# Optimization experiments

Measured on AMD Instinct MI355X. Metric: run time of the kernel, lower is better.

Reference implementation:

```python
import jax, jax.numpy as jnp
import numpy as np

H = 16          # num_attention_heads
D = 1024        # hidden_size
HD = D // H     # attention_head_size = 64


def setup_inputs() -> dict:
    key = jax.random.key(0)
    ks = jax.random.split(key, 9)
    s = 1.0 / np.sqrt(D)
    return {
        "hidden_states": jax.random.normal(ks[0], (4, 1024, D), jnp.float32),
        "encoder_hidden_states": jax.random.normal(ks[1], (4, 1024, D), jnp.float32),
        "attention_mask": jnp.zeros((4, 1, 1, 2048), jnp.float32),
        "Wq": jax.random.normal(ks[2], (D, D), jnp.float32) * s,
        "bq": jnp.zeros((D,), jnp.float32),
        "Wk": jax.random.normal(ks[3], (D, D), jnp.float32) * s,
        "bk": jnp.zeros((D,), jnp.float32),
        "Wv": jax.random.normal(ks[4], (D, D), jnp.float32) * s,
        "bv": jnp.zeros((D,), jnp.float32),
    }


def _split_heads(x):
    # [B, S, D] -> [B, H, S, HD]
    B, S, _ = x.shape
    return x.reshape(B, S, H, HD).transpose(0, 2, 1, 3)


def reference(hidden_states, encoder_hidden_states, attention_mask, Wq, bq, Wk, bk, Wv, bv):
    # KV over concat(encoder, decoder); Q over decoder hidden states only.
    all_hidden = jnp.concatenate([encoder_hidden_states, hidden_states], axis=1)  # [B, Skv, D]
    q = _split_heads(hidden_states @ Wq + bq)        # [B, H, Sq, HD]
    k = _split_heads(all_hidden @ Wk + bk)           # [B, H, Skv, HD]
    v = _split_heads(all_hidden @ Wv + bv)           # [B, H, Skv, HD]

    scores = jnp.einsum("bhqd,bhkd->bhqk", q, k) / np.sqrt(HD).astype(np.float32)
    scores = scores + attention_mask                 # additive mask, broadcast
    probs = jax.nn.softmax(scores, axis=-1)          # dropout p=0 (eval)
    ctx = jnp.einsum("bhqk,bhkd->bhqd", probs, v)    # [B, H, Sq, HD]
    B, _, Sq, _ = ctx.shape
    return ctx.transpose(0, 2, 1, 3).reshape(B, Sq, D)
```

## Files before the change

### kernel.cpp

```cpp
#include <hip/hip_runtime.h>


typedef _Float16 f16;
typedef __attribute__((ext_vector_type(4))) _Float16 half4;
typedef __attribute__((ext_vector_type(8))) _Float16 half8;
typedef __attribute__((ext_vector_type(4))) float floatx4;
typedef __attribute__((ext_vector_type(16))) float floatx16;
typedef __attribute__((ext_vector_type(4))) unsigned int uint4v;

#define GLOAD16(gp, lp)                                                        \
    __builtin_amdgcn_global_load_lds(                                          \
        (const __attribute__((address_space(1))) void*)(gp),                   \
        (__attribute__((address_space(3))) void*)(lp), 16, 0, 0)

__global__ void prep_kernel(const float* __restrict__ hid, const float* __restrict__ enc,
                            const float* __restrict__ Wq, const float* __restrict__ Wk,
                            const float* __restrict__ Wv, f16* __restrict__ Wtq,
                            f16* __restrict__ Wtk, f16* __restrict__ Wtv,
                            f16* __restrict__ Aall) {
    int bid = blockIdx.x, tid = threadIdx.x;
    if (bid < 3072) {
        __shared__ float tile[32][33];
        int z = bid >> 10, xy = bid & 1023;
        const float* W = (z == 0) ? Wq : (z == 1) ? Wk : Wv;
        f16* Wt = (z == 0) ? Wtq : (z == 1) ? Wtk : Wtv;
        int n0 = (xy & 31) * 32, k0 = (xy >> 5) * 32;
        int tx = tid & 31, ty = tid >> 5;
        #pragma unroll
        for (int i = 0; i < 32; i += 8)
            tile[ty + i][tx] = W[(k0 + ty + i) * 1024 + n0 + tx];
        __syncthreads();
        #pragma unroll
        for (int i = 0; i < 32; i += 8)
            Wt[(n0 + ty + i) * 1024 + k0 + tx] = (f16)tile[tx][ty + i];
    } else {
        int t = (bid - 3072) * 256 + tid;
        int rowg = t >> 7, col = (t & 127) * 8;
        int b = rowg >> 11, r = rowg & 2047;
        const float* src = (r < 1024 ? enc + ((size_t)b * 1024 + r) * 1024
                                     : hid + ((size_t)b * 1024 + (r - 1024)) * 1024) + col;
        float4 v0 = *(const float4*)src, v1 = *(const float4*)(src + 4);
        half8 o;
        o[0] = (f16)v0.x; o[1] = (f16)v0.y; o[2] = (f16)v0.z; o[3] = (f16)v0.w;
        o[4] = (f16)v1.x; o[5] = (f16)v1.y; o[6] = (f16)v1.z; o[7] = (f16)v1.w;
        *(half8*)(Aall + (size_t)rowg * 1024 + col) = o;
    }
}

__launch_bounds__(256)
__global__ void qkv_gemm(const f16* __restrict__ Aall,
                         const f16* __restrict__ Wtq, const f16* __restrict__ Wtk,
                         const f16* __restrict__ Wtv,
                         const float* __restrict__ bq, const float* __restrict__ bk,
                         const float* __restrict__ bv,
                         f16* __restrict__ Qw, f16* __restrict__ Kw, f16* __restrict__ Vtw) {
    int mode = blockIdx.z;
    if (mode == 0 && blockIdx.x >= 32) return;
    __shared__ f16 As[2][128 * 32];
    __shared__ f16 Bs[2][128 * 32];

    const f16* Wt = (mode == 0) ? Wtq : (mode == 1) ? Wtk : Wtv;
    const float* bias = (mode == 0) ? bq : (mode == 1) ? bk : bv;
    f16* out = (mode == 0) ? Qw : (mode == 1) ? Kw : Vtw;

    int tid = threadIdx.x;
    int m0 = blockIdx.x * 128, n0 = blockIdx.y * 128;
    int wid = tid >> 6, lane = tid & 63;
    int wm = (wid >> 1) * 64, wn = (wid & 1) * 64;
    int lr = lane & 15, lg = lane >> 4;

    floatx4 acc[4][4];
    #pragma unroll
    for (int i = 0; i < 4; i++)
        #pragma unroll
        for (int j = 0; j < 4; j++) acc[i][j] = (floatx4)(0.f);

    int trow = tid >> 2, tcol = (tid & 3) * 8;
    const f16 *a0g, *a1g;
    {
        int mA0 = m0 + trow, mA1 = mA0 + 64;
        if (mode == 0) {
            int b0 = mA0 >> 10, b1 = mA1 >> 10;
            a0g = Aall + ((size_t)(b0 * 2048 + 1024 + (mA0 & 1023))) * 1024 + tcol;
            a1g = Aall + ((size_t)(b1 * 2048 + 1024 + (mA1 & 1023))) * 1024 + tcol;
        } else {
            a0g = Aall + (size_t)mA0 * 1024 + tcol;
            a1g = Aall + (size_t)mA1 * 1024 + tcol;
        }
    }
    const f16* b0g = Wt + (size_t)(n0 + trow) * 1024 + tcol;
    const f16* b1g = Wt + (size_t)(n0 + trow + 64) * 1024 + tcol;

    GLOAD16(a0g, &As[0][tid * 8]);
    GLOAD16(a1g, &As[0][tid * 8 + 2048]);
    GLOAD16(b0g, &Bs[0][tid * 8]);
    GLOAD16(b1g, &Bs[0][tid * 8 + 2048]);
    __syncthreads();

    int cur = 0;
    for (int k0 = 0; k0 < 1024; k0 += 32) {
        if (k0 < 992) {
            int nx = cur ^ 1;
            GLOAD16(a0g + k0 + 32, &As[nx][tid * 8]);
            GLOAD16(a1g + k0 + 32, &As[nx][tid * 8 + 2048]);
            GLOAD16(b0g + k0 + 32, &Bs[nx][tid * 8]);
            GLOAD16(b1g + k0 + 32, &Bs[nx][tid * 8 + 2048]);
        }
        half8 a[4], bf[4];
        #pragma unroll
        for (int i = 0; i < 4; i++)
            a[i] = *(const half8*)&As[cur][(wm + i * 16 + lr) * 32 + lg * 8];
        #pragma unroll
        for (int j = 0; j < 4; j++)
            bf[j] = *(const half8*)&Bs[cur][(wn + j * 16 + lr) * 32 + lg * 8];
        __builtin_amdgcn_s_setprio(1);
        #pragma unroll
        for (int i = 0; i < 4; i++)
            #pragma unroll
            for (int j = 0; j < 4; j++)
                acc[i][j] = __builtin_amdgcn_mfma_f32_16x16x32_f16(a[i], bf[j], acc[i][j], 0, 0, 0);
        __builtin_amdgcn_s_setprio(0);
        __syncthreads();
        cur ^= 1;
    }

    if (mode == 2) {
        #pragma unroll
        for (int i = 0; i < 4; i++) {
            int mbase = m0 + wm + i * 16 + lg * 4;
            int b = mbase >> 11, s = mbase & 2047;
            #pragma unroll
            for (int j = 0; j < 4; j++) {
                int n = n0 + wn + j * 16 + lr;
                int h = n >> 6, d = n & 63;
                float bv = bias[n];
                half4 w;
                #pragma unroll
                for (int r = 0; r < 4; r++) w[r] = (f16)(acc[i][j][r] + bv);
                *(half4*)(out + ((size_t)((b * 16 + h) * 64 + d)) * 2048 + s) = w;
            }
        }
    } else {
        int Sout = (mode == 0) ? 1024 : 2048;
        #pragma unroll
        for (int i = 0; i < 4; i++) {
            int mbase = m0 + wm + i * 16 + lg * 4;
            #pragma unroll
            for (int j = 0; j < 4; j++) {
                int n = n0 + wn + j * 16 + lr;
                int h = n >> 6, d = n & 63;
                float bv = bias[n];
                #pragma unroll
                for (int r = 0; r < 4; r++) {
                    int m = mbase + r;
                    int b = (mode == 0) ? (m >> 10) : (m >> 11);
                    int s = (mode == 0) ? (m & 1023) : (m & 2047);
                    out[((size_t)(b * 16 + h) * Sout + s) * 64 + d] = (f16)(acc[i][j][r] + bv);
                }
            }
        }
    }
}

__device__ inline half8 pack_swap(float s0, float s1, float s2, float s3,
                                  float s4, float s5, float s6, float s7) {
    unsigned a0 = __builtin_bit_cast(unsigned, __builtin_amdgcn_cvt_pkrtz(s0, s1));
    unsigned b0 = __builtin_bit_cast(unsigned, __builtin_amdgcn_cvt_pkrtz(s4, s5));
    unsigned a1 = __builtin_bit_cast(unsigned, __builtin_amdgcn_cvt_pkrtz(s2, s3));
    unsigned b1 = __builtin_bit_cast(unsigned, __builtin_amdgcn_cvt_pkrtz(s6, s7));
    asm("v_permlane32_swap_b32 %0, %1" : "+v"(a0), "+v"(b0));
    asm("v_permlane32_swap_b32 %0, %1" : "+v"(a1), "+v"(b1));
    uint4v w = {a0, a1, b0, b1};
    return __builtin_bit_cast(half8, w);
}

__device__ inline half8 pack_noswap(float s0, float s1, float s2, float s3,
                                    float s4, float s5, float s6, float s7) {
    unsigned w0 = __builtin_bit_cast(unsigned, __builtin_amdgcn_cvt_pkrtz(s0, s1));
    unsigned w1 = __builtin_bit_cast(unsigned, __builtin_amdgcn_cvt_pkrtz(s2, s3));
    unsigned w2 = __builtin_bit_cast(unsigned, __builtin_amdgcn_cvt_pkrtz(s4, s5));
    unsigned w3 = __builtin_bit_cast(unsigned, __builtin_amdgcn_cvt_pkrtz(s6, s7));
    uint4v w = {w0, w1, w2, w3};
    return __builtin_bit_cast(half8, w);
}

__launch_bounds__(256)
__global__ void attn_kernel(const f16* __restrict__ Q, const f16* __restrict__ K,
                            const f16* __restrict__ Vt, const float* __restrict__ mask,
                            float* __restrict__ out) {
    __shared__ f16 Kt[2][64 * 72];
    __shared__ f16 Vtt[2][64 * 72];
    __shared__ float maskLds[2048];

    const float LOG2E = 1.4426950408889634f;
    int tid = threadIdx.x;
    int wid = tid >> 6, lane = tid & 63;
    int l31 = lane & 31, l5 = lane >> 5;

    int bid = blockIdx.x + 8 * blockIdx.y;
    int xcd = bid & 7, w = bid >> 3;
    int bh = xcd * 8 + (w >> 3);
    int xblk = w & 7;
    int b = bh >> 4;
    int q = xblk * 128 + wid * 32 + l31;

    half8 pa, pcode;
    #pragma unroll
    for (int j = 0; j < 8; j++) { pa[j] = (f16)0; pcode[j] = (f16)(8 * l5 + j); }
    if (l31 < 16 && (l31 >> 3) == l5) pa[l31 & 7] = (f16)1;
    floatx16 pd = __builtin_amdgcn_mfma_f32_32x32x16_f16(pa, pcode, (floatx16)0.f, 0, 0, 0);
    float r4 = __shfl(pd[0], 32);
    bool twoblk = (r4 > 6.0f);

    const float* maskp = mask + b * 2048;
    for (int i = tid; i < 512; i += 256) {
        float4 mv = ((const float4*)maskp)[i];
        mv.x = mv.x * LOG2E - 8.0f; mv.y = mv.y * LOG2E - 8.0f;
        mv.z = mv.z * LOG2E - 8.0f; mv.w = mv.w * LOG2E - 8.0f;
        ((float4*)maskLds)[i] = mv;
    }

    const f16* qrow = Q + ((size_t)bh * 1024 + q) * 64;
    half8 qf[4];
    if (!twoblk) {
        #pragma unroll
        for (int ks = 0; ks < 4; ks++)
            qf[ks] = *(const half8*)(qrow + ks * 16 + l5 * 8);
    } else {
        #pragma unroll
        for (int ks = 0; ks < 4; ks++) {
            half4 lo = *(const half4*)(qrow + ks * 16 + 4 * l5);
            half4 hi = *(const half4*)(qrow + ks * 16 + 8 + 4 * l5);
            qf[ks][0] = lo[0]; qf[ks][1] = lo[1]; qf[ks][2] = lo[2]; qf[ks][3] = lo[3];
            qf[ks][4] = hi[0]; qf[ks][5] = hi[1]; qf[ks][6] = hi[2]; qf[ks][7] = hi[3];
        }
    }
    const f16 qs = (f16)(0.125f * 1.4426950408889634f);
    #pragma unroll
    for (int ks = 0; ks < 4; ks++)
        #pragma unroll
        for (int x = 0; x < 8; x++) qf[ks][x] *= qs;

    half8 aones;
    #pragma unroll
    for (int j = 0; j < 8; j++) aones[j] = (l31 == 0) ? (f16)1 : (f16)0;

    floatx16 o0 = (floatx16)0.f, o1 = (floatx16)0.f, o2 = (floatx16)0.f;

    int sr = tid >> 2, sc = (tid & 3) * 16;
    const f16* Ksrc = K + ((size_t)bh * 2048 + sr) * 64 + sc;
    const f16* Vsrc = Vt + ((size_t)(bh * 64 + sr)) * 2048 + sc;

    half8 rk0 = *(const half8*)(Ksrc);
    half8 rk1 = *(const half8*)(Ksrc + 8);
    half8 rv0 = *(const half8*)(Vsrc);
    half8 rv1 = *(const half8*)(Vsrc + 8);
    *(half8*)&Kt[0][sr * 72 + sc]      = rk0;
    *(half8*)&Kt[0][sr * 72 + sc + 8]  = rk1;
    *(half8*)&Vtt[0][sr * 72 + sc]     = rv0;
    *(half8*)&Vtt[0][sr * 72 + sc + 8] = rv1;
    rk0 = *(const half8*)(Ksrc + (size_t)64 * 64);
    rk1 = *(const half8*)(Ksrc + (size_t)64 * 64 + 8);
    rv0 = *(const half8*)(Vsrc + 64);
    rv1 = *(const half8*)(Vsrc + 64 + 8);
    __syncthreads();

    int cur = 0;
    for (int kv0 = 0; kv0 < 2048; kv0 += 64) {
        if (kv0 < 2048 - 64) {
            int nx = cur ^ 1;
            *(half8*)&Kt[nx][sr * 72 + sc]      = rk0;
            *(half8*)&Kt[nx][sr * 72 + sc + 8]  = rk1;
            *(half8*)&Vtt[nx][sr * 72 + sc]     = rv0;
            *(half8*)&Vtt[nx][sr * 72 + sc + 8] = rv1;
            if (kv0 < 2048 - 128) {
                rk0 = *(const half8*)(Ksrc + (size_t)(kv0 + 128) * 64);
                rk1 = *(const half8*)(Ksrc + (size_t)(kv0 + 128) * 64 + 8);
                rv0 = *(const half8*)(Vsrc + kv0 + 128);
                rv1 = *(const half8*)(Vsrc + kv0 + 128 + 8);
            }
        }

        floatx16 sf0, sf1;
        #pragma unroll
        for (int g = 0; g < 4; g++) {
            float4 mk0 = *(const float4*)&maskLds[kv0 + 8 * g + 4 * l5];
            float4 mk1 = *(const float4*)&maskLds[kv0 + 32 + 8 * g + 4 * l5];
            #pragma unroll
            for (int i = 0; i < 4; i++) {
                sf0[4 * g + i] = ((const float*)&mk0)[i];
                sf1[4 * g + i] = ((const float*)&mk1)[i];
            }
        }

        __builtin_amdgcn_s_setprio(1);
        #pragma unroll
        for (int ks = 0; ks < 4; ks++) {
            half8 k0 = *(const half8*)&Kt[cur][l31 * 72 + ks * 16 + l5 * 8];
            half8 k1 = *(const half8*)&Kt[cur][(32 + l31) * 72 + ks * 16 + l5 * 8];
            sf0 = __builtin_amdgcn_mfma_f32_32x32x16_f16(k0, qf[ks], sf0, 0, 0, 0);
            sf1 = __builtin_amdgcn_mfma_f32_32x32x16_f16(k1, qf[ks], sf1, 0, 0, 0);
        }
        __builtin_amdgcn_s_setprio(0);

        #pragma unroll
        for (int r = 0; r < 16; r++) {
            sf0[r] = exp2f(sf0[r]);
            sf1[r] = exp2f(sf1[r]);
        }

        half8 pb[4];
        if (!twoblk) {
            pb[0] = pack_swap(sf0[0], sf0[1], sf0[2], sf0[3], sf0[4], sf0[5], sf0[6], sf0[7]);
            pb[1] = pack_swap(sf0[8], sf0[9], sf0[10], sf0[11], sf0[12], sf0[13], sf0[14], sf0[15]);
            pb[2] = pack_swap(sf1[0], sf1[1], sf1[2], sf1[3], sf1[4], sf1[5], sf1[6], sf1[7]);
            pb[3] = pack_swap(sf1[8], sf1[9], sf1[10], sf1[11], sf1[12], sf1[13], sf1[14], sf1[15]);
        } else {
            pb[0] = pack_noswap(sf0[0], sf0[1], sf0[2], sf0[3], sf0[4], sf0[5], sf0[6], sf0[7]);
            pb[1] = pack_noswap(sf0[8], sf0[9], sf0[10], sf0[11], sf0[12], sf0[13], sf0[14], sf0[15]);
            pb[2] = pack_noswap(sf1[0], sf1[1], sf1[2], sf1[3], sf1[4], sf1[5], sf1[6], sf1[7]);
            pb[3] = pack_noswap(sf1[8], sf1[9], sf1[10], sf1[11], sf1[12], sf1[13], sf1[14], sf1[15]);
        }

        __builtin_amdgcn_s_setprio(1);
        #pragma unroll
        for (int kb = 0; kb < 4; kb++) {
            half8 v0 = *(const half8*)&Vtt[cur][l31 * 72 + kb * 16 + l5 * 8];
            half8 v1 = *(const half8*)&Vtt[cur][(32 + l31) * 72 + kb * 16 + l5 * 8];
            o0 = __builtin_amdgcn_mfma_f32_32x32x16_f16(v0, pb[kb], o0, 0, 0, 0);
            o1 = __builtin_amdgcn_mfma_f32_32x32x16_f16(v1, pb[kb], o1, 0, 0, 0);
            o2 = __builtin_amdgcn_mfma_f32_32x32x16_f16(aones, pb[kb], o2, 0, 0, 0);
        }
        __builtin_amdgcn_s_setprio(0);

        asm volatile("s_waitcnt lgkmcnt(0)" ::: "memory");
        __builtin_amdgcn_sched_barrier(0);
        __builtin_amdgcn_s_barrier();
        cur ^= 1;
    }

    float l_all = __shfl(o2[0], l31);
    int h = bh & 15;
    float inv = 1.f / l_all;
    float* orow = out + ((size_t)(b * 1024 + q)) * 1024 + h * 64;
    #pragma unroll
    for (int g = 0; g < 4; g++) {
        float4 r0 = {o0[4 * g] * inv, o0[4 * g + 1] * inv, o0[4 * g + 2] * inv, o0[4 * g + 3] * inv};
        float4 r1 = {o1[4 * g] * inv, o1[4 * g + 1] * inv, o1[4 * g + 2] * inv, o1[4 * g + 3] * inv};
        *(float4*)&orow[8 * g + 4 * l5]      = r0;
        *(float4*)&orow[32 + 8 * g + 4 * l5] = r1;
    }
}

extern "C" void kernel_launch(void* const* d_in, const int* in_sizes, int n_in,
                              void* d_out, int out_size, void* d_ws, size_t ws_size,
                              hipStream_t stream) {
    const float* hid  = (const float*)d_in[0];
    const float* enc  = (const float*)d_in[1];
    const float* mask = (const float*)d_in[2];
    const float* Wq   = (const float*)d_in[3];
    const float* bq   = (const float*)d_in[4];
    const float* Wk   = (const float*)d_in[5];
    const float* bk   = (const float*)d_in[6];
    const float* Wv   = (const float*)d_in[7];
    const float* bv   = (const float*)d_in[8];
    float* out = (float*)d_out;

    char* ws = (char*)d_ws;
    f16* Wtq  = (f16*)(ws + ((size_t)0 << 20));
    f16* Wtk  = (f16*)(ws + ((size_t)2 << 20));
    f16* Wtv  = (f16*)(ws + ((size_t)4 << 20));
    f16* Aall = (f16*)(ws + ((size_t)6 << 20));
    f16* Qw   = (f16*)(ws + ((size_t)22 << 20));
    f16* Kw   = (f16*)(ws + ((size_t)30 << 20));
    f16* Vtw  = (f16*)(ws + ((size_t)46 << 20));

    prep_kernel<<<7168, 256, 0, stream>>>(hid, enc, Wq, Wk, Wv, Wtq, Wtk, Wtv, Aall);

    qkv_gemm<<<dim3(64, 8, 3), 256, 0, stream>>>(Aall, Wtq, Wtk, Wtv, bq, bk, bv, Qw, Kw, Vtw);

    attn_kernel<<<dim3(8, 64), 256, 0, stream>>>(Qw, Kw, Vtw, mask, out);
}
```

Baseline: 146.7 us.

## Swizzle QKV GEMM LDS tiles and keep two loads in flight with explicit waitcnt

Reworks the QKV projection GEMM main loop to unroll by two over separate LDS buffers. Loads are issued two stages ahead, with hand-placed s_waitcnt vmcnt and raw barriers replacing __syncthreads, so one tile's global-to-LDS copy overlaps compute on the other. It also XOR-swizzles the 16-byte column chunk on both the LDS write and read sides to cut LDS bank conflicts on the fragment reads. The manual wait counts rely on exact ordering of memory operations and could expose races if the compiler reorders them.

```diff
diff --git a/kernel.cpp b/kernel.cpp
--- a/kernel.cpp
+++ b/kernel.cpp
@@ -56,8 +56,10 @@
                          f16* __restrict__ Qw, f16* __restrict__ Kw, f16* __restrict__ Vtw) {
     int mode = blockIdx.z;
     if (mode == 0 && blockIdx.x >= 32) return;
-    __shared__ f16 As[2][128 * 32];
-    __shared__ f16 Bs[2][128 * 32];
+    __shared__ f16 As0[128 * 32];
+    __shared__ f16 Bs0[128 * 32];
+    __shared__ f16 As1[128 * 32];
+    __shared__ f16 Bs1[128 * 32];
 
     const f16* Wt = (mode == 0) ? Wtq : (mode == 1) ? Wtk : Wtv;
     const float* bias = (mode == 0) ? bq : (mode == 1) ? bk : bv;
@@ -75,7 +77,8 @@
         #pragma unroll
         for (int j = 0; j < 4; j++) acc[i][j] = (floatx4)(0.f);
 
-    int trow = tid >> 2, tcol = (tid & 3) * 8;
+    int trow = tid >> 2;
+    int tcol = (((tid & 3) ^ ((tid >> 3) & 3))) * 8;
     const f16 *a0g, *a1g;
     {
         int mA0 = m0 + trow, mA1 = mA0 + 64;
@@ -91,38 +94,66 @@
     const f16* b0g = Wt + (size_t)(n0 + trow) * 1024 + tcol;
     const f16* b1g = Wt + (size_t)(n0 + trow + 64) * 1024 + tcol;
 
-    GLOAD16(a0g, &As[0][tid * 8]);
-    GLOAD16(a1g, &As[0][tid * 8 + 2048]);
-    GLOAD16(b0g, &Bs[0][tid * 8]);
-    GLOAD16(b1g, &Bs[0][tid * 8 + 2048]);
-    __syncthreads();
-
-    int cur = 0;
-    for (int k0 = 0; k0 < 1024; k0 += 32) {
-        if (k0 < 992) {
-            int nx = cur ^ 1;
-            GLOAD16(a0g + k0 + 32, &As[nx][tid * 8]);
-            GLOAD16(a1g + k0 + 32, &As[nx][tid * 8 + 2048]);
-            GLOAD16(b0g + k0 + 32, &Bs[nx][tid * 8]);
-            GLOAD16(b1g + k0 + 32, &Bs[nx][tid * 8 + 2048]);
-        }
-        half8 a[4], bf[4];
-        #pragma unroll
-        for (int i = 0; i < 4; i++)
-            a[i] = *(const half8*)&As[cur][(wm + i * 16 + lr) * 32 + lg * 8];
-        #pragma unroll
-        for (int j = 0; j < 4; j++)
-            bf[j] = *(const half8*)&Bs[cur][(wn + j * 16 + lr) * 32 + lg * 8];
-        __builtin_amdgcn_s_setprio(1);
-        #pragma unroll
-        for (int i = 0; i < 4; i++)
-            #pragma unroll
-            for (int j = 0; j < 4; j++)
-                acc[i][j] = __builtin_amdgcn_mfma_f32_16x16x32_f16(a[i], bf[j], acc[i][j], 0, 0, 0);
-        __builtin_amdgcn_s_setprio(0);
-        __syncthreads();
-        cur ^= 1;
-    }
+    int rcol = (lg ^ ((lr >> 1) & 3)) * 8;
+
+    GLOAD16(a0g, &As0[tid * 8]);
+    GLOAD16(a1g, &As0[tid * 8 + 2048]);
+    GLOAD16(b0g, &Bs0[tid * 8]);
+    GLOAD16(b1g, &Bs0[tid * 8 + 2048]);
+    GLOAD16(a0g + 32, &As1[tid * 8]);
+    GLOAD16(a1g + 32, &As1[tid * 8 + 2048]);
+    GLOAD16(b0g + 32, &Bs1[tid * 8]);
+    GLOAD16(b1g + 32, &Bs1[tid * 8 + 2048]);
+    asm volatile("s_waitcnt vmcnt(4)" ::: "memory");
+    __builtin_amdgcn_s_barrier();
+
+    #define QKV_COMPUTE(Abuf, Bbuf)                                                       \
+        {                                                                                 \
+            half8 a[4], bf[4];                                                            \
+            _Pragma("unroll")                                                             \
+            for (int i = 0; i < 4; i++)                                                   \
+                a[i] = *(const half8*)&Abuf[(wm + i * 16 + lr) * 32 + rcol];              \
+            _Pragma("unroll")                                                             \
+            for (int j = 0; j < 4; j++)                                                   \
+                bf[j] = *(const half8*)&Bbuf[(wn + j * 16 + lr) * 32 + rcol];             \
+            __builtin_amdgcn_s_setprio(1);                                                \
+            _Pragma("unroll")                                                             \
+            for (int i = 0; i < 4; i++)                                                   \
+                _Pragma("unroll")                                                         \
+                for (int j = 0; j < 4; j++)                                               \
+                    acc[i][j] = __builtin_amdgcn_mfma_f32_16x16x32_f16(a[i], bf[j],       \
+                                                                      acc[i][j], 0, 0, 0);\
+            __builtin_amdgcn_s_setprio(0);                                                \
+        }
+
+    for (int k0 = 0; k0 < 1024; k0 += 64) {
+        QKV_COMPUTE(As0, Bs0);
+        asm volatile("s_waitcnt lgkmcnt(0)" ::: "memory");
+        __builtin_amdgcn_s_barrier();
+        if (k0 + 64 < 1024) {
+            GLOAD16(a0g + k0 + 64, &As0[tid * 8]);
+            GLOAD16(a1g + k0 + 64, &As0[tid * 8 + 2048]);
+            GLOAD16(b0g + k0 + 64, &Bs0[tid * 8]);
+            GLOAD16(b1g + k0 + 64, &Bs0[tid * 8 + 2048]);
+            asm volatile("s_waitcnt vmcnt(4)" ::: "memory");
+        } else {
+            asm volatile("s_waitcnt vmcnt(0)" ::: "memory");
+        }
+        __builtin_amdgcn_s_barrier();
+
+        QKV_COMPUTE(As1, Bs1);
+        asm volatile("s_waitcnt lgkmcnt(0)" ::: "memory");
+        __builtin_amdgcn_s_barrier();
+        if (k0 + 96 < 1024) {
+            GLOAD16(a0g + k0 + 96, &As1[tid * 8]);
+            GLOAD16(a1g + k0 + 96, &As1[tid * 8 + 2048]);
+            GLOAD16(b0g + k0 + 96, &Bs1[tid * 8]);
+            GLOAD16(b1g + k0 + 96, &Bs1[tid * 8 + 2048]);
+            asm volatile("s_waitcnt vmcnt(4)" ::: "memory");
+            __builtin_amdgcn_s_barrier();
+        }
+    }
+    #undef QKV_COMPUTE
 
     if (mode == 2) {
         #pragma unroll
```

Measured after the change: 143.6 us. 2.1% less time.
